# Kernel optimization log

Hardware: AMD Instinct MI355X
Metric: run time of the kernel (lower is better)

Reference implementation:

```python
import jax, jax.numpy as jnp
import numpy as np

ITERS = 10   # self.iters
REG = 0.1    # self.reg
EPS = 1e-12  # F.normalize eps


def setup_inputs() -> dict:
    key = jax.random.key(0)
    k1, k2 = jax.random.split(key)
    b, n_s, h = 64, 512, 1024
    x = jax.random.normal(k1, (b, n_s, h), dtype=jnp.float32)
    y = jax.random.normal(k2, (b, n_s, h), dtype=jnp.float32)
    return {"x": x, "y": y}


def _l2_normalize(t):
    n = jnp.sqrt(jnp.sum(t * t, axis=-1, keepdims=True))
    return t / jnp.maximum(n, EPS)


def reference(x, y):
    # CosineScorer.score(x, y, get_diag=False) with temperature=1
    xn = _l2_normalize(x)
    yn = _l2_normalize(y)
    scores = jnp.einsum('bmh,bnh->bmn', xn, yn)  # (b, n_s, n_s)
    b, m, n = scores.shape

    # uniform log marginals: -log(n_s)
    log_mu = jnp.full((b, m), -jnp.log(jnp.float32(m)), dtype=scores.dtype)
    log_nu = jnp.full((b, n), -jnp.log(jnp.float32(n)), dtype=scores.dtype)

    # log_ipot: iterative proximal point OT in log space
    A = scores / jnp.float32(REG)

    def step(carry, _):
        v, T = carry
        Q = A + T                                              # (b, m, n)
        u = log_mu - jax.nn.logsumexp(Q + v[:, None, :], axis=2)
        v_new = log_nu - jax.nn.logsumexp(Q + u[:, :, None], axis=1)
        T_new = Q + u[:, :, None] + v_new[:, None, :]
        return (v_new, T_new), None

    init = (log_nu, jnp.zeros_like(scores))
    (_, T), _ = jax.lax.scan(step, init, None, length=ITERS)

    matching = jnp.exp(T)
    return jnp.sum(scores * matching, axis=(1, 2))  # (b,)
```

## Files before the change

### kernel.cpp

```cpp
#include <hip/hip_runtime.h>
#include <hip/hip_fp16.h>

#define NB 64
#define NS 512
#define NH 1024
#define NITERS 10

#define LOG_INV_NS (-6.238324625039508f)

using half8 = _Float16 __attribute__((ext_vector_type(8)));
using f32x4 = float __attribute__((ext_vector_type(4)));

__global__ __launch_bounds__(512) void gemm_fused(
    const float* __restrict__ x, const float* __restrict__ y,
    _Float16* __restrict__ Sh) {
  __shared__ _Float16 As[2][256][72];
  __shared__ _Float16 Bs[2][256][72];
  __shared__ float invA[256], invB[256];

  int blk = blockIdx.x;
  int b = blk & 63;
  int tile = blk >> 6;
  int tm = (tile >> 1) * 256, tn = (tile & 1) * 256;
  int tid = threadIdx.x;
  int wid = tid >> 6, lane = tid & 63;
  int wr = (wid >> 2) * 128;
  int wc = (wid & 3) * 64;
  int fr = lane & 15, fq = lane >> 4;

  int srow = tid >> 1;
  int skh = (tid & 1) * 16;
  const float* xb = x + ((size_t)b * NS + tm + srow) * NH + skh;
  const float* yb = y + ((size_t)b * NS + tn + srow) * NH + skh;

  f32x4 acc[8][4] = {};
  float4 rx[4], ry[4];
  float sqx = 0.f, sqy = 0.f;

#define GLOAD(K0)                                                     \
  do {                                                                \
    const float4* px = (const float4*)(xb + (K0));                    \
    const float4* py = (const float4*)(yb + (K0));                    \
    rx[0] = px[0]; rx[1] = px[1]; rx[2] = px[2]; rx[3] = px[3];       \
    ry[0] = py[0]; ry[1] = py[1]; ry[2] = py[2]; ry[3] = py[3];       \
  } while (0)

#define CAST_WRITE(BUF, COL)                                          \
  do {                                                                \
    alignas(16) _Float16 ta[16];                                      \
    alignas(16) _Float16 tb[16];                                      \
    _Pragma("unroll") for (int j = 0; j < 4; ++j) {                   \
      float4 v = rx[j];                                               \
      ta[4 * j + 0] = (_Float16)v.x; ta[4 * j + 1] = (_Float16)v.y;   \
      ta[4 * j + 2] = (_Float16)v.z; ta[4 * j + 3] = (_Float16)v.w;   \
      sqx += v.x * v.x + v.y * v.y + v.z * v.z + v.w * v.w;           \
    }                                                                 \
    _Pragma("unroll") for (int j = 0; j < 4; ++j) {                   \
      float4 v = ry[j];                                               \
      tb[4 * j + 0] = (_Float16)v.x; tb[4 * j + 1] = (_Float16)v.y;   \
      tb[4 * j + 2] = (_Float16)v.z; tb[4 * j + 3] = (_Float16)v.w;   \
      sqy += v.x * v.x + v.y * v.y + v.z * v.z + v.w * v.w;           \
    }                                                                 \
    *(half8*)&As[BUF][srow][(COL) + skh + 0] = *(half8*)&ta[0];       \
    *(half8*)&As[BUF][srow][(COL) + skh + 8] = *(half8*)&ta[8];       \
    *(half8*)&Bs[BUF][srow][(COL) + skh + 0] = *(half8*)&tb[0];       \
    *(half8*)&Bs[BUF][srow][(COL) + skh + 8] = *(half8*)&tb[8];       \
  } while (0)

  GLOAD(0);
  CAST_WRITE(0, 0);
  GLOAD(32);
  CAST_WRITE(0, 32);
  GLOAD(64);
  asm volatile("s_waitcnt lgkmcnt(0)" ::: "memory");
  __builtin_amdgcn_sched_barrier(0);
  __builtin_amdgcn_s_barrier();
  __builtin_amdgcn_sched_barrier(0);

  for (int s = 0; s < 16; ++s) {
    int cur = s & 1;
    {
      half8 bf[4];
#pragma unroll
      for (int j = 0; j < 4; ++j)
        bf[j] = *(const half8*)&Bs[cur][wc + 16 * j + fr][8 * fq];
#pragma unroll
      for (int i = 0; i < 8; ++i) {
        half8 af = *(const half8*)&As[cur][wr + 16 * i + fr][8 * fq];
#pragma unroll
        for (int j = 0; j < 4; ++j)
          acc[i][j] = __builtin_amdgcn_mfma_f32_16x16x32_f16(af, bf[j], acc[i][j], 0, 0, 0);
      }
    }
    if (s < 15) {
      CAST_WRITE(cur ^ 1, 0);
      GLOAD((s + 1) * 64 + 32);
    }
    {
      half8 bf[4];
#pragma unroll
      for (int j = 0; j < 4; ++j)
        bf[j] = *(const half8*)&Bs[cur][wc + 16 * j + fr][32 + 8 * fq];
#pragma unroll
      for (int i = 0; i < 8; ++i) {
        half8 af = *(const half8*)&As[cur][wr + 16 * i + fr][32 + 8 * fq];
#pragma unroll
        for (int j = 0; j < 4; ++j)
          acc[i][j] = __builtin_amdgcn_mfma_f32_16x16x32_f16(af, bf[j], acc[i][j], 0, 0, 0);
      }
    }
    if (s < 15) {
      CAST_WRITE(cur ^ 1, 32);
      if (s < 14) GLOAD((s + 2) * 64);
    }
    asm volatile("s_waitcnt lgkmcnt(0)" ::: "memory");
    __builtin_amdgcn_sched_barrier(0);
    __builtin_amdgcn_s_barrier();
    __builtin_amdgcn_sched_barrier(0);
  }
#undef GLOAD
#undef CAST_WRITE

  sqx += __shfl_xor(sqx, 1, 64);
  sqy += __shfl_xor(sqy, 1, 64);
  if ((tid & 1) == 0) {
    invA[srow] = 1.0f / fmaxf(sqrtf(sqx), 1e-12f);
    invB[srow] = 1.0f / fmaxf(sqrtf(sqy), 1e-12f);
  }
  __syncthreads();

  _Float16* Sb = Sh + (size_t)b * NS * NS;
#pragma unroll
  for (int i = 0; i < 8; ++i)
#pragma unroll
    for (int j = 0; j < 4; ++j) {
      int rr = wr + 16 * i + 4 * fq;
      int cc = wc + 16 * j + fr;
      float ib = invB[cc];
#pragma unroll
      for (int p = 0; p < 4; ++p)
        Sb[(size_t)(tm + rr + p) * NS + tn + cc] =
            (_Float16)(acc[i][j][p] * invA[rr + p] * ib);
    }
}

__global__ __launch_bounds__(256) void u_first_kernel(
    const _Float16* __restrict__ Sh, float* __restrict__ U, float f) {
  int blk = blockIdx.x;
  int bs = blk & 7, rest = blk >> 3;
  int rowgrp = rest & 31, bq = rest >> 5;
  int b = bq * 8 + bs;
  int t = threadIdx.x;
  int w = t >> 6, l = t & 63;
  int m0 = rowgrp * 16 + w * 4;
  const _Float16* Sb = Sh + ((size_t)b * NS + m0) * NS + 8 * l;
  float sum[4] = {0.f, 0.f, 0.f, 0.f};
#pragma unroll
  for (int k = 0; k < 4; ++k) {
    half8 hv = *(const half8*)(Sb + (size_t)k * NS);
#pragma unroll
    for (int e = 0; e < 8; ++e) sum[k] += __expf(fmaf(f, (float)hv[e], LOG_INV_NS));
  }
#pragma unroll
  for (int o = 32; o; o >>= 1) {
#pragma unroll
    for (int k = 0; k < 4; ++k) sum[k] += __shfl_xor(sum[k], o, 64);
  }
  if (l == 0) {
#pragma unroll
    for (int k = 0; k < 4; ++k)
      U[b * NS + m0 + k] = LOG_INV_NS - __logf(sum[k]);
  }
}

__global__ __launch_bounds__(256) void p_kernel(
    const _Float16* __restrict__ Sh, const float* __restrict__ Ufirst,
    float* __restrict__ V, float* __restrict__ rowpart,
    float f, float fnext, int first, int last, float* __restrict__ outPart) {
  __shared__ float Ul[NS];
  __shared__ float partC[64][33];
  __shared__ float partD[64][33];
  __shared__ float redC[4][33];
  __shared__ float redD[4][33];
  __shared__ float Wl[32];
  __shared__ float partR[NS][5];

  int blk = blockIdx.x;
  int b = blk & 63;
  int ng = blk >> 6;
  int t = threadIdx.x;
  int w = t >> 6, l = t & 63;

  if (first) {
    Ul[t] = Ufirst[b * NS + t];
    Ul[t + 256] = Ufirst[b * NS + t + 256];
  } else {
    const float* rp = rowpart + (size_t)b * 16 * NS;
    float s0 = 0.f, s1 = 0.f;
#pragma unroll
    for (int k = 0; k < 16; ++k) {
      s0 += rp[k * NS + t];
      s1 += rp[k * NS + t + 256];
    }
    Ul[t] = LOG_INV_NS - __logf(s0);
    Ul[t + 256] = LOG_INV_NS - __logf(s1);
  }
  __syncthreads();

  int oct = t & 3;
  int mc = t >> 2;
  const _Float16* Sbc = Sh + (size_t)b * NS * NS + (size_t)(mc * 8) * NS + ng * 32 + oct * 8;
  half8 hv[8];
#pragma unroll
  for (int i = 0; i < 8; ++i) hv[i] = *(const half8*)(Sbc + (size_t)i * NS);

  float c[8] = {}, d[8] = {};
  if (!last) {
#pragma unroll
    for (int i = 0; i < 8; ++i) {
      float um = Ul[mc * 8 + i];
#pragma unroll
      for (int e = 0; e < 8; ++e)
        c[e] += __expf(fmaf(f, (float)hv[i][e], um));
    }
  } else {
#pragma unroll
    for (int i = 0; i < 8; ++i) {
      float um = Ul[mc * 8 + i];
#pragma unroll
      for (int e = 0; e < 8; ++e) {
        float sv = (float)hv[i][e];
        float ev = __expf(fmaf(f, sv, um));
        c[e] += ev;
        d[e] = fmaf(sv, ev, d[e]);
      }
    }
  }
#pragma unroll
  for (int e = 0; e < 8; ++e) {
    partC[mc][oct * 8 + e] = c[e];
    if (last) partD[mc][oct * 8 + e] = d[e];
  }
  __syncthreads();
  {
    int ci = t & 31, seg = t >> 5;
    float cc = 0.f, dd = 0.f;
#pragma unroll
    for (int k = 0; k < 8; ++k) {
      cc += partC[seg * 8 + k][ci];
      if (last) dd += partD[seg * 8 + k][ci];
    }
    cc += __shfl_xor(cc, 32, 64);
    if (last) dd += __shfl_xor(dd, 32, 64);
    if (l < 32) { redC[w][l] = cc; if (last) redD[w][l] = dd; }
  }
  __syncthreads();
  if (t < 32) {
    float cc = redC[0][t] + redC[1][t] + redC[2][t] + redC[3][t];
    if (!last) {
      float vnew = LOG_INV_NS - __logf(cc);
      int n = b * NS + ng * 32 + t;
      float vold = first ? 0.f : V[n];
      V[n] = vnew;
      Wl[t] = 2.f * vnew - vold;
    } else {
      float dd = redD[0][t] + redD[1][t] + redD[2][t] + redD[3][t];
      float r = dd / cc;
      r += __shfl_xor(r, 16, 64);
      r += __shfl_xor(r, 8, 64);
      r += __shfl_xor(r, 4, 64);
      r += __shfl_xor(r, 2, 64);
      r += __shfl_xor(r, 1, 64);
      if (t == 0) outPart[b * 16 + ng] = r * (1.0f / (float)NS);
    }
  }
  if (last) return;
  __syncthreads();

  float wl[8];
#pragma unroll
  for (int e = 0; e < 8; ++e) wl[e] = Wl[oct * 8 + e];
#pragma unroll
  for (int i = 0; i < 8; ++i) {
    float s = 0.f;
#pragma unroll
    for (int e = 0; e < 8; ++e)
      s += __expf(fmaf(fnext, (float)hv[i][e], wl[e]));
    partR[mc * 8 + i][oct] = s;
  }
  __syncthreads();
  {
    float* rp = rowpart + ((size_t)b * 16 + ng) * NS;
    float q0 = partR[t][0] + partR[t][1] + partR[t][2] + partR[t][3];
    float q1 = partR[t + 256][0] + partR[t + 256][1] + partR[t + 256][2] + partR[t + 256][3];
    rp[t] = q0;
    rp[t + 256] = q1;
  }
}

__global__ void combine_kernel(const float* __restrict__ outPart, float* __restrict__ out) {
  int b = threadIdx.x;
  float s = 0.f;
#pragma unroll
  for (int k = 0; k < 16; ++k) s += outPart[b * 16 + k];
  out[b] = s;
}

extern "C" void kernel_launch(void* const* d_in, const int* in_sizes, int n_in,
                              void* d_out, int out_size, void* d_ws, size_t ws_size,
                              hipStream_t stream) {
  (void)in_sizes; (void)n_in; (void)out_size; (void)ws_size;
  const float* x = (const float*)d_in[0];
  const float* y = (const float*)d_in[1];
  float* out = (float*)d_out;

  char* ws = (char*)d_ws;
  _Float16* Sh = (_Float16*)ws;
  float* fregion = (float*)(ws + (size_t)NB * NS * NS * 2);
  float* U = fregion;
  float* V = U + NB * NS;
  float* outPart = V + NB * NS;
  float* rowpart = outPart + 1024;

  gemm_fused<<<256, 512, 0, stream>>>(x, y, Sh);
  u_first_kernel<<<2048, 256, 0, stream>>>(Sh, U, 10.0f);

  for (int t = 1; t <= NITERS; ++t) {
    p_kernel<<<1024, 256, 0, stream>>>(Sh, U, V, rowpart,
                                       10.0f * (float)t, 10.0f * (float)(t + 1),
                                       t == 1 ? 1 : 0, t == NITERS ? 1 : 0,
                                       outPart);
  }
  combine_kernel<<<1, 64, 0, stream>>>(outPart, out);
}
```

Measured before the change: 178.7 us.

## Fuse first row-logsumexp into GEMM epilogue and switch to base-2 exponentials

Removes the separate u_first kernel by computing per-row partial exp sums in the GEMM epilogue, writing per-tile partials to a workspace buffer that the first p_kernel iteration combines. All exp/log calls are rewritten in base 2 (exp2f/log2f) with the scale constants pre-multiplied by log2(e), which saves a multiply per exponential. The cost is extra epilogue work and shuffles in the GEMM, plus the first-row sums now come from fp32 scores instead of the fp16-rounded ones.

```diff
diff --git a/kernel.cpp b/kernel.cpp
--- a/kernel.cpp
+++ b/kernel.cpp
@@ -6,17 +6,19 @@
 #define NH 1024
 #define NITERS 10
 
-#define LOG_INV_NS (-6.238324625039508f)
+#define LOG2_INV_NS (-9.0f)
+#define LOG2E 1.4426950408889634f
 
 using half8 = _Float16 __attribute__((ext_vector_type(8)));
 using f32x4 = float __attribute__((ext_vector_type(4)));
 
 __global__ __launch_bounds__(512) void gemm_fused(
     const float* __restrict__ x, const float* __restrict__ y,
-    _Float16* __restrict__ Sh) {
+    _Float16* __restrict__ Sh, float* __restrict__ upartG) {
   __shared__ _Float16 As[2][256][72];
   __shared__ _Float16 Bs[2][256][72];
   __shared__ float invA[256], invB[256];
+  __shared__ float upartL[4][256];
 
   int blk = blockIdx.x;
   int b = blk & 63;
@@ -129,54 +131,45 @@
   }
   __syncthreads();
 
+  const float F2 = 10.0f * LOG2E;
   _Float16* Sb = Sh + (size_t)b * NS * NS;
 #pragma unroll
-  for (int i = 0; i < 8; ++i)
+  for (int i = 0; i < 8; ++i) {
+    float rs[4] = {0.f, 0.f, 0.f, 0.f};
 #pragma unroll
     for (int j = 0; j < 4; ++j) {
-      int rr = wr + 16 * i + 4 * fq;
-      int cc = wc + 16 * j + fr;
-      float ib = invB[cc];
+      int ccol = wc + 16 * j + fr;
+      float ib = invB[ccol];
+#pragma unroll
+      for (int p = 0; p < 4; ++p) {
+        int rr = wr + 16 * i + 4 * fq + p;
+        float sval = acc[i][j][p] * invA[rr] * ib;
+        Sb[(size_t)(tm + rr) * NS + tn + ccol] = (_Float16)sval;
+        rs[p] += exp2f(fmaf(F2, sval, LOG2_INV_NS));
+      }
+    }
+#pragma unroll
+    for (int mask = 1; mask <= 8; mask <<= 1) {
+#pragma unroll
+      for (int p = 0; p < 4; ++p) rs[p] += __shfl_xor(rs[p], mask, 64);
+    }
+    if (fr == 0) {
 #pragma unroll
       for (int p = 0; p < 4; ++p)
-        Sb[(size_t)(tm + rr + p) * NS + tn + cc] =
-            (_Float16)(acc[i][j][p] * invA[rr + p] * ib);
-    }
+        upartL[wid & 3][wr + 16 * i + 4 * fq + p] = rs[p];
+    }
+  }
+  __syncthreads();
+  if (tid < 256) {
+    float s = upartL[0][tid] + upartL[1][tid] + upartL[2][tid] + upartL[3][tid];
+    upartG[(((size_t)b * 2 + (tile >> 1)) * 2 + (tile & 1)) * 256 + tid] = s;
+  }
 }
 
-__global__ __launch_bounds__(256) void u_first_kernel(
-    const _Float16* __restrict__ Sh, float* __restrict__ U, float f) {
-  int blk = blockIdx.x;
-  int bs = blk & 7, rest = blk >> 3;
-  int rowgrp = rest & 31, bq = rest >> 5;
-  int b = bq * 8 + bs;
-  int t = threadIdx.x;
-  int w = t >> 6, l = t & 63;
-  int m0 = rowgrp * 16 + w * 4;
-  const _Float16* Sb = Sh + ((size_t)b * NS + m0) * NS + 8 * l;
-  float sum[4] = {0.f, 0.f, 0.f, 0.f};
-#pragma unroll
-  for (int k = 0; k < 4; ++k) {
-    half8 hv = *(const half8*)(Sb + (size_t)k * NS);
-#pragma unroll
-    for (int e = 0; e < 8; ++e) sum[k] += __expf(fmaf(f, (float)hv[e], LOG_INV_NS));
-  }
-#pragma unroll
-  for (int o = 32; o; o >>= 1) {
-#pragma unroll
-    for (int k = 0; k < 4; ++k) sum[k] += __shfl_xor(sum[k], o, 64);
-  }
-  if (l == 0) {
-#pragma unroll
-    for (int k = 0; k < 4; ++k)
-      U[b * NS + m0 + k] = LOG_INV_NS - __logf(sum[k]);
-  }
-}
-
 __global__ __launch_bounds__(256) void p_kernel(
-    const _Float16* __restrict__ Sh, const float* __restrict__ Ufirst,
+    const _Float16* __restrict__ Sh, const float* __restrict__ upartG,
     float* __restrict__ V, float* __restrict__ rowpart,
-    float f, float fnext, int first, int last, float* __restrict__ outPart) {
+    float f2, float fnext2, int first, int last, float* __restrict__ outPart) {
   __shared__ float Ul[NS];
   __shared__ float partC[64][33];
   __shared__ float partD[64][33];
@@ -192,8 +185,11 @@
   int w = t >> 6, l = t & 63;
 
   if (first) {
-    Ul[t] = Ufirst[b * NS + t];
-    Ul[t + 256] = Ufirst[b * NS + t + 256];
+    const float* up = upartG + (size_t)b * 1024;
+    float s0 = up[t] + up[256 + t];
+    float s1 = up[512 + t] + up[768 + t];
+    Ul[t] = LOG2_INV_NS - log2f(s0);
+    Ul[t + 256] = LOG2_INV_NS - log2f(s1);
   } else {
     const float* rp = rowpart + (size_t)b * 16 * NS;
     float s0 = 0.f, s1 = 0.f;
@@ -202,8 +198,8 @@
       s0 += rp[k * NS + t];
       s1 += rp[k * NS + t + 256];
     }
-    Ul[t] = LOG_INV_NS - __logf(s0);
-    Ul[t + 256] = LOG_INV_NS - __logf(s1);
+    Ul[t] = LOG2_INV_NS - log2f(s0);
+    Ul[t + 256] = LOG2_INV_NS - log2f(s1);
   }
   __syncthreads();
 
@@ -221,7 +217,7 @@
       float um = Ul[mc * 8 + i];
 #pragma unroll
       for (int e = 0; e < 8; ++e)
-        c[e] += __expf(fmaf(f, (float)hv[i][e], um));
+        c[e] += exp2f(fmaf(f2, (float)hv[i][e], um));
     }
   } else {
 #pragma unroll
@@ -230,7 +226,7 @@
 #pragma unroll
       for (int e = 0; e < 8; ++e) {
         float sv = (float)hv[i][e];
-        float ev = __expf(fmaf(f, sv, um));
+        float ev = exp2f(fmaf(f2, sv, um));
         c[e] += ev;
         d[e] = fmaf(sv, ev, d[e]);
       }
@@ -258,11 +254,11 @@
   if (t < 32) {
     float cc = redC[0][t] + redC[1][t] + redC[2][t] + redC[3][t];
     if (!last) {
-      float vnew = LOG_INV_NS - __logf(cc);
+      float vnew2 = LOG2_INV_NS - log2f(cc);
       int n = b * NS + ng * 32 + t;
-      float vold = first ? 0.f : V[n];
-      V[n] = vnew;
-      Wl[t] = 2.f * vnew - vold;
+      float vold2 = first ? 0.f : V[n];
+      V[n] = vnew2;
+      Wl[t] = 2.f * vnew2 - vold2;
     } else {
       float dd = redD[0][t] + redD[1][t] + redD[2][t] + redD[3][t];
       float r = dd / cc;
@@ -285,7 +281,7 @@
     float s = 0.f;
 #pragma unroll
     for (int e = 0; e < 8; ++e)
-      s += __expf(fmaf(fnext, (float)hv[i][e], wl[e]));
+      s += exp2f(fmaf(fnext2, (float)hv[i][e], wl[e]));
     partR[mc * 8 + i][oct] = s;
   }
   __syncthreads();
@@ -317,17 +313,17 @@
   char* ws = (char*)d_ws;
   _Float16* Sh = (_Float16*)ws;
   float* fregion = (float*)(ws + (size_t)NB * NS * NS * 2);
-  float* U = fregion;
-  float* V = U + NB * NS;
+  float* V = fregion;
   float* outPart = V + NB * NS;
   float* rowpart = outPart + 1024;
-
-  gemm_fused<<<256, 512, 0, stream>>>(x, y, Sh);
-  u_first_kernel<<<2048, 256, 0, stream>>>(Sh, U, 10.0f);
+  float* upartG = rowpart + (size_t)NB * 16 * NS;
+
+  gemm_fused<<<256, 512, 0, stream>>>(x, y, Sh, upartG);
 
   for (int t = 1; t <= NITERS; ++t) {
-    p_kernel<<<1024, 256, 0, stream>>>(Sh, U, V, rowpart,
-                                       10.0f * (float)t, 10.0f * (float)(t + 1),
+    p_kernel<<<1024, 256, 0, stream>>>(Sh, upartG, V, rowpart,
+                                       10.0f * LOG2E * (float)t,
+                                       10.0f * LOG2E * (float)(t + 1),
                                        t == 1 ? 1 : 0, t == NITERS ? 1 : 0,
                                        outPart);
   }
```

After: 206.5 us. +15.5%, slower.
